# Kernel tuning notes

Measured on AMD Instinct MI355X. Metric: run time of the kernel, lower is better.

## Reference

```python
import jax, jax.numpy as jnp
import numpy as np

N, E, K = 10000, 160000, 5
K3 = K ** 3  # 125 spline kernel entries (kernel_size=5, dim=3)
NUM_CLASSES = 6890
# 8 corner combinations of the degree-1 open B-spline in 3 dims
_COMBOS = jnp.asarray(np.array([[i, j, k] for i in (0, 1) for j in (0, 1) for k in (0, 1)], dtype=np.int32))


def spline_basis(pseudo):
    # pseudo: [E,3] in [0,1]; degree-1 open B-spline, kernel_size K per dim
    p = pseudo * (K - 1)
    lo_f = jnp.floor(p)
    frac = p - lo_f                                   # [E,3]
    lo = jnp.clip(lo_f.astype(jnp.int32), 0, K - 1)    # [E,3]
    hi = jnp.minimum(lo + 1, K - 1)
    w = jnp.stack([1.0 - frac, frac], axis=-1)         # [E,3,2]
    idx = jnp.stack([lo, hi], axis=-1)                 # [E,3,2]
    c = _COMBOS                                        # [8,3]
    b = w[:, 0, c[:, 0]] * w[:, 1, c[:, 1]] * w[:, 2, c[:, 2]]          # [E,8]
    flat = idx[:, 0, c[:, 0]] + K * idx[:, 1, c[:, 1]] + K * K * idx[:, 2, c[:, 2]]  # [E,8]
    return b, flat


def spline_conv(x, src, dst, b, flat, W, root, bias):
    # x: [N,in], W: [K3,in,out], root: [in,out], bias: [out]
    xW = jnp.einsum('ni,kio->nko', x, W)               # [N,K3,out]
    gathered = xW[src[:, None], flat]                  # [E,8,out]
    msg = jnp.einsum('es,eso->eo', b, gathered)        # [E,out]
    agg = jax.ops.segment_sum(msg, dst, num_segments=N)
    deg = jax.ops.segment_sum(jnp.ones((msg.shape[0],), msg.dtype), dst, num_segments=N)
    agg = agg / jnp.maximum(deg, 1.0)[:, None]         # mean aggregation
    return agg + x @ root + bias


def setup_inputs() -> dict:
    key = jax.random.key(0)
    ks = jax.random.split(key, 24)
    s = 0.1
    x = jax.random.normal(ks[0], (N, 1), jnp.float32)
    edge_index = jax.random.randint(ks[1], (2, E), 0, N)
    pseudo = jax.random.uniform(ks[2], (E, 3), dtype=jnp.float32)
    W1 = jax.random.normal(ks[3], (K3, 1, 32), jnp.float32) * s
    root1 = jax.random.normal(ks[4], (1, 32), jnp.float32) * s
    b1 = jnp.zeros((32,), jnp.float32)
    W2 = jax.random.normal(ks[5], (K3, 32, 64), jnp.float32) * s
    root2 = jax.random.normal(ks[6], (32, 64), jnp.float32) * s
    b2 = jnp.zeros((64,), jnp.float32)
    Ws = jax.random.normal(ks[7], (4, K3, 64, 64), jnp.float32) * s  # convs 3-6
    roots = jax.random.normal(ks[8], (4, 64, 64), jnp.float32) * s
    bs = jnp.zeros((4, 64), jnp.float32)
    lin1_w = jax.random.normal(ks[9], (64, 256), jnp.float32) * s
    lin1_b = jnp.zeros((256,), jnp.float32)
    lin2_w = jax.random.normal(ks[10], (256, NUM_CLASSES), jnp.float32) * s
    lin2_b = jnp.zeros((NUM_CLASSES,), jnp.float32)
    return {'x': x, 'edge_index': edge_index, 'pseudo': pseudo,
            'W1': W1, 'root1': root1, 'b1': b1,
            'W2': W2, 'root2': root2, 'b2': b2,
            'Ws': Ws, 'roots': roots, 'bs': bs,
            'lin1_w': lin1_w, 'lin1_b': lin1_b, 'lin2_w': lin2_w, 'lin2_b': lin2_b}


def reference(x, edge_index, pseudo, W1, root1, b1, W2, root2, b2, Ws, roots, bs,
              lin1_w, lin1_b, lin2_w, lin2_b):
    src, dst = edge_index[0], edge_index[1]
    b, flat = spline_basis(pseudo)
    h = jax.nn.elu(spline_conv(x, src, dst, b, flat, W1, root1, b1))
    h = jax.nn.elu(spline_conv(h, src, dst, b, flat, W2, root2, b2))
    for l in range(4):  # convs 3-6, fixed layer loop
        h = jax.nn.elu(spline_conv(h, src, dst, b, flat, Ws[l], roots[l], bs[l]))
    h = jax.nn.elu(h @ lin1_w + lin1_b)
    # dropout is identity in eval mode
    logits = h @ lin2_w + lin2_b
    return jax.nn.log_softmax(logits, axis=-1)
```

## Files before the change

### kernel.cpp

```cpp
#include <hip/hip_runtime.h>
#include <math.h>

#define Nn 10000
#define Ee 160000
#define NPB 40
#define NBLK 250
#define NKER 125
#define NBUCK (NBLK * NKER)
#define KCHUNK 32

__global__ __launch_bounds__(256) void basis_kernel(const float* __restrict__ pseudo,
                                                    float* __restrict__ bw,
                                                    int* __restrict__ fl)
{
    int e = blockIdx.x * 256 + threadIdx.x;
    if (e >= Ee) return;
    float p0 = pseudo[e * 3 + 0] * 4.f;
    float p1 = pseudo[e * 3 + 1] * 4.f;
    float p2 = pseudo[e * 3 + 2] * 4.f;
    float f0 = floorf(p0), f1 = floorf(p1), f2 = floorf(p2);
    float fr0 = p0 - f0, fr1 = p1 - f1, fr2 = p2 - f2;
    int lo0 = (int)f0; lo0 = lo0 < 0 ? 0 : (lo0 > 4 ? 4 : lo0);
    int lo1 = (int)f1; lo1 = lo1 < 0 ? 0 : (lo1 > 4 ? 4 : lo1);
    int lo2 = (int)f2; lo2 = lo2 < 0 ? 0 : (lo2 > 4 ? 4 : lo2);
    int hi0 = lo0 + 1 > 4 ? 4 : lo0 + 1;
    int hi1 = lo1 + 1 > 4 ? 4 : lo1 + 1;
    int hi2 = lo2 + 1 > 4 ? 4 : lo2 + 1;
#pragma unroll
    for (int s = 0; s < 8; ++s) {
        int c0 = (s >> 2) & 1, c1 = (s >> 1) & 1, c2 = s & 1;
        float b = (c0 ? fr0 : 1.f - fr0) * (c1 ? fr1 : 1.f - fr1) * (c2 ? fr2 : 1.f - fr2);
        int f = (c0 ? hi0 : lo0) + 5 * (c1 ? hi1 : lo1) + 25 * (c2 ? hi2 : lo2);
        bw[e * 8 + s] = b;
        fl[e * 8 + s] = f;
    }
}

__global__ __launch_bounds__(256) void deg_kernel(const int* __restrict__ dst, int* __restrict__ degi)
{
    int e = blockIdx.x * 256 + threadIdx.x;
    if (e >= Ee) return;
    atomicAdd(&degi[dst[e]], 1);
}

__global__ __launch_bounds__(256) void invdeg_kernel(const int* __restrict__ degi, float* __restrict__ invdeg)
{
    int n = blockIdx.x * 256 + threadIdx.x;
    if (n >= Nn) return;
    int d = degi[n];
    invdeg[n] = 1.f / (float)(d > 0 ? d : 1);
}

__global__ __launch_bounds__(256) void hist_kernel(const int* __restrict__ dst, const int* __restrict__ fl,
                                                   int* __restrict__ hist)
{
    int t = blockIdx.x * 256 + threadIdx.x;
    if (t >= Ee * 8) return;
    int e = t >> 3;
    int key = (dst[e] / NPB) * NKER + fl[t];
    atomicAdd(&hist[key], 1);
}

__global__ __launch_bounds__(1024) void scan_kernel(const int* __restrict__ hist, int* __restrict__ boff)
{
    const int T = 1024;
    const int per = (NBUCK + T - 1) / T;
    int t = threadIdx.x;
    int beg = t * per;
    int end = beg + per; if (end > NBUCK) end = NBUCK;
    int s = 0;
    for (int i = beg; i < end && i < NBUCK; ++i) s += hist[i];
    __shared__ int tmp[1024];
    tmp[t] = s;
    __syncthreads();
    for (int o2 = 1; o2 < 1024; o2 <<= 1) {
        int v = (t >= o2) ? tmp[t - o2] : 0;
        __syncthreads();
        tmp[t] += v;
        __syncthreads();
    }
    int run = tmp[t] - s;
    for (int i = beg; i < end && i < NBUCK; ++i) { boff[i] = run; run += hist[i]; }
    if (t == T - 1) boff[NBUCK] = run;
}

__global__ __launch_bounds__(256) void fill_kernel(const int* __restrict__ srcA, const int* __restrict__ dstA,
                                                   const float* __restrict__ bw, const int* __restrict__ fl,
                                                   int* __restrict__ cursor, uint2* __restrict__ recs)
{
    int t = blockIdx.x * 256 + threadIdx.x;
    if (t >= Ee * 8) return;
    int e = t >> 3;
    int d = dstA[e];
    int key = (d / NPB) * NKER + fl[t];
    int pos = atomicAdd(&cursor[key], 1);
    unsigned meta = (unsigned)srcA[e] | ((unsigned)(d % NPB) << 16);
    recs[pos] = make_uint2(meta, __float_as_uint(bw[t]));
}

template <int CIN, int COUT>
__global__ __launch_bounds__(256) void conv_pairs_kernel(const uint2* __restrict__ recs,
                                                         const int* __restrict__ boff,
                                                         const float* __restrict__ xin,
                                                         const float* __restrict__ W,
                                                         float* __restrict__ agg)
{
    __shared__ float aggl[NPB * COUT];
    const int blk = blockIdx.x;
    for (int idx = threadIdx.x; idx < NPB * COUT; idx += 256) aggl[idx] = 0.f;
    __syncthreads();

    const int lane = threadIdx.x & 63;
    const int wid  = threadIdx.x >> 6;
    const int o    = lane;

    int k0 = blockIdx.y * KCHUNK;
    int k1 = k0 + KCHUNK; if (k1 > NKER) k1 = NKER;

    for (int k = k0; k < k1; ++k) {
        int bidx = blk * NKER + k;
        int pb = boff[bidx], pe = boff[bidx + 1];
        if (pb >= pe) continue;
        float wreg[CIN];
#pragma unroll
        for (int i = 0; i < CIN; ++i)
            wreg[i] = (o < COUT) ? W[(k * CIN + i) * COUT + o] : 0.f;

        for (int p = pb + wid; p < pe; p += 4) {
            uint2 r = recs[p];
            unsigned meta = (unsigned)__builtin_amdgcn_readfirstlane((int)r.x);
            float wt = __uint_as_float(r.y);
            int src = (int)(meta & 0xFFFFu);
            int dl  = (int)(meta >> 16);
            const float* xs = xin + src * CIN;
            float m0 = 0.f, m1 = 0.f, m2 = 0.f, m3 = 0.f;
            if (CIN >= 4) {
#pragma unroll
                for (int i = 0; i < CIN; i += 4) {
                    m0 += xs[i + 0] * wreg[i + 0];
                    m1 += xs[i + 1] * wreg[i + 1];
                    m2 += xs[i + 2] * wreg[i + 2];
                    m3 += xs[i + 3] * wreg[i + 3];
                }
            } else {
#pragma unroll
                for (int i = 0; i < CIN; ++i) m0 += xs[i] * wreg[i];
            }
            float m = (m0 + m1) + (m2 + m3);
            if (o < COUT) atomicAdd(&aggl[dl * COUT + o], wt * m);
        }
    }
    __syncthreads();
    for (int idx = threadIdx.x; idx < NPB * COUT; idx += 256) {
        int n = blk * NPB + idx / COUT;
        if (n < Nn) atomicAdd(&agg[n * COUT + (idx % COUT)], aggl[idx]);
    }
}

template <int CIN, int COUT>
__global__ __launch_bounds__(256) void epilogue_kernel(const float* __restrict__ agg,
                                                       const float* __restrict__ xin,
                                                       const float* __restrict__ root,
                                                       const float* __restrict__ bias,
                                                       const float* __restrict__ invdeg,
                                                       float* __restrict__ out)
{
    int idx = blockIdx.x * 256 + threadIdx.x;
    int n = idx / COUT, o = idx % COUT;
    if (n >= Nn) return;
    float r0 = 0.f, r1 = 0.f;
#pragma unroll
    for (int i = 0; i < CIN; i += 2) {
        r0 += xin[n * CIN + i] * root[i * COUT + o];
        if (CIN > 1) r1 += xin[n * CIN + i + 1] * root[(i + 1) * COUT + o];
    }
    float v = agg[n * COUT + o] * invdeg[n] + r0 + r1 + bias[o];
    out[n * COUT + o] = v > 0.f ? v : expm1f(v);
}

__global__ __launch_bounds__(256) void lin1_kernel(const float* __restrict__ h,
                                                   const float* __restrict__ w1,
                                                   const float* __restrict__ b1,
                                                   float* __restrict__ out)
{
    int n = blockIdx.x;
    __shared__ float hl[64];
    if (threadIdx.x < 64) hl[threadIdx.x] = h[n * 64 + threadIdx.x];
    __syncthreads();
    int j = threadIdx.x;
    float a0 = b1[j], a1 = 0.f, a2 = 0.f, a3 = 0.f;
#pragma unroll
    for (int i = 0; i < 64; i += 4) {
        a0 += hl[i + 0] * w1[(i + 0) * 256 + j];
        a1 += hl[i + 1] * w1[(i + 1) * 256 + j];
        a2 += hl[i + 2] * w1[(i + 2) * 256 + j];
        a3 += hl[i + 3] * w1[(i + 3) * 256 + j];
    }
    float acc = (a0 + a1) + (a2 + a3);
    out[n * 256 + j] = acc > 0.f ? acc : expm1f(acc);
}

#define LNT 32
__global__ __launch_bounds__(256) void lin2_kernel(const float* __restrict__ h,
                                                   const float* __restrict__ w2,
                                                   const float* __restrict__ b2,
                                                   float* __restrict__ out)
{
    __shared__ float hT[256 * LNT];
    int n0 = blockIdx.x * LNT;
    int j0 = blockIdx.y * 1024;
    for (int idx = threadIdx.x; idx < 256 * LNT; idx += 256) {
        int i = idx & 255, nl = idx >> 8;
        hT[i * LNT + nl] = (n0 + nl < Nn) ? h[(n0 + nl) * 256 + i] : 0.f;
    }
    __syncthreads();

    int j[4];
#pragma unroll
    for (int c = 0; c < 4; ++c) j[c] = j0 + (int)threadIdx.x + 256 * c;

    float acc[4][LNT];
#pragma unroll
    for (int c = 0; c < 4; ++c)
#pragma unroll
        for (int nl = 0; nl < LNT; ++nl) acc[c][nl] = 0.f;

    for (int i = 0; i < 256; ++i) {
        float wv[4];
#pragma unroll
        for (int c = 0; c < 4; ++c)
            wv[c] = (j[c] < 6890) ? w2[i * 6890 + j[c]] : 0.f;
        const float4* hp = (const float4*)&hT[i * LNT];
#pragma unroll
        for (int q = 0; q < LNT / 4; ++q) {
            float4 h4 = hp[q];
#pragma unroll
            for (int c = 0; c < 4; ++c) {
                acc[c][q * 4 + 0] += wv[c] * h4.x;
                acc[c][q * 4 + 1] += wv[c] * h4.y;
                acc[c][q * 4 + 2] += wv[c] * h4.z;
                acc[c][q * 4 + 3] += wv[c] * h4.w;
            }
        }
    }
#pragma unroll
    for (int c = 0; c < 4; ++c) {
        if (j[c] >= 6890) continue;
        float bb = b2[j[c]];
        for (int nl = 0; nl < LNT; ++nl) {
            int n = n0 + nl;
            if (n < Nn) out[(size_t)n * 6890 + j[c]] = acc[c][nl] + bb;
        }
    }
}

__global__ __launch_bounds__(1024) void lsm_kernel(float* __restrict__ out)
{
    int row = blockIdx.x;
    float* p = out + (size_t)row * 6890;
    __shared__ float red[16];
    int tid = threadIdx.x, lane = tid & 63, wid = tid >> 6;

    float m = -3.4e38f;
    for (int jj = tid; jj < 6890; jj += 1024) m = fmaxf(m, p[jj]);
#pragma unroll
    for (int off = 32; off > 0; off >>= 1) m = fmaxf(m, __shfl_down(m, off));
    if (lane == 0) red[wid] = m;
    __syncthreads();
    if (tid == 0) {
        float mm = red[0];
        for (int w = 1; w < 16; ++w) mm = fmaxf(mm, red[w]);
        red[0] = mm;
    }
    __syncthreads();
    m = red[0];
    __syncthreads();

    float s = 0.f;
    for (int jj = tid; jj < 6890; jj += 1024) s += expf(p[jj] - m);
#pragma unroll
    for (int off = 32; off > 0; off >>= 1) s += __shfl_down(s, off);
    if (lane == 0) red[wid] = s;
    __syncthreads();
    if (tid == 0) {
        float ss = 0.f;
        for (int w = 1; w < 16; ++w) ss += red[w];
        red[0] += ss;
    }
    __syncthreads();
    float lse = m + logf(red[0]);
    for (int jj = tid; jj < 6890; jj += 1024) p[jj] -= lse;
}

extern "C" void kernel_launch(void* const* d_in, const int* in_sizes, int n_in,
                              void* d_out, int out_size, void* d_ws, size_t ws_size,
                              hipStream_t stream)
{
    const float* x      = (const float*)d_in[0];
    const int*   ei     = (const int*)d_in[1];
    const float* pseudo = (const float*)d_in[2];
    const float* W1     = (const float*)d_in[3];
    const float* root1  = (const float*)d_in[4];
    const float* b1     = (const float*)d_in[5];
    const float* W2     = (const float*)d_in[6];
    const float* root2  = (const float*)d_in[7];
    const float* b2     = (const float*)d_in[8];
    const float* Ws     = (const float*)d_in[9];
    const float* roots  = (const float*)d_in[10];
    const float* bs     = (const float*)d_in[11];
    const float* l1w    = (const float*)d_in[12];
    const float* l1b    = (const float*)d_in[13];
    const float* l2w    = (const float*)d_in[14];
    const float* l2b    = (const float*)d_in[15];
    float* out = (float*)d_out;

    const int* srcA = ei;
    const int* dstA = ei + Ee;

    char* base = (char*)d_ws;
    size_t off = 0;
    auto carve = [&](size_t bytes) -> void* {
        void* p = base + off;
        off += (bytes + 255) & ~(size_t)255;
        return p;
    };
    float* bw     = (float*)carve((size_t)Ee * 8 * 4);
    int*   fl     = (int*)carve((size_t)Ee * 8 * 4);
    int*   hist   = (int*)carve((size_t)NBUCK * 4);
    int*   boff   = (int*)carve((size_t)(NBUCK + 1) * 4);
    int*   cursor = (int*)carve((size_t)NBUCK * 4);
    uint2* recs   = (uint2*)carve((size_t)Ee * 8 * 8);
    int*   degi   = (int*)carve((size_t)Nn * 4);
    float* invdeg = (float*)carve((size_t)Nn * 4);
    float* agg    = (float*)carve((size_t)Nn * 64 * 4);
    float* hA     = (float*)carve((size_t)Nn * 64 * 4);
    float* hB     = (float*)carve((size_t)Nn * 64 * 4);
    float* h256   = (float*)carve((size_t)Nn * 256 * 4);
    (void)ws_size; (void)n_in; (void)in_sizes; (void)out_size;

    hipMemsetAsync(hist, 0, (size_t)NBUCK * 4, stream);
    hipMemsetAsync(degi, 0, (size_t)Nn * 4, stream);

    basis_kernel<<<(Ee + 255) / 256, 256, 0, stream>>>(pseudo, bw, fl);
    deg_kernel<<<(Ee + 255) / 256, 256, 0, stream>>>(dstA, degi);
    invdeg_kernel<<<(Nn + 255) / 256, 256, 0, stream>>>(degi, invdeg);
    hist_kernel<<<(Ee * 8 + 255) / 256, 256, 0, stream>>>(dstA, fl, hist);
    scan_kernel<<<1, 1024, 0, stream>>>(hist, boff);
    hipMemcpyAsync(cursor, boff, (size_t)NBUCK * 4, hipMemcpyDeviceToDevice, stream);
    fill_kernel<<<(Ee * 8 + 255) / 256, 256, 0, stream>>>(srcA, dstA, bw, fl, cursor, recs);

    const dim3 cgrid(NBLK, (NKER + KCHUNK - 1) / KCHUNK);

    hipMemsetAsync(agg, 0, (size_t)Nn * 64 * 4, stream);
    conv_pairs_kernel<1, 32><<<cgrid, 256, 0, stream>>>(recs, boff, x, W1, agg);
    epilogue_kernel<1, 32><<<(Nn * 32 + 255) / 256, 256, 0, stream>>>(agg, x, root1, b1, invdeg, hA);

    hipMemsetAsync(agg, 0, (size_t)Nn * 64 * 4, stream);
    conv_pairs_kernel<32, 64><<<cgrid, 256, 0, stream>>>(recs, boff, hA, W2, agg);
    epilogue_kernel<32, 64><<<(Nn * 64 + 255) / 256, 256, 0, stream>>>(agg, hA, root2, b2, invdeg, hB);

    float* cin = hB;
    float* cot = hA;
    for (int l = 0; l < 4; ++l) {
        hipMemsetAsync(agg, 0, (size_t)Nn * 64 * 4, stream);
        conv_pairs_kernel<64, 64><<<cgrid, 256, 0, stream>>>(recs, boff, cin, Ws + (size_t)l * 125 * 64 * 64, agg);
        epilogue_kernel<64, 64><<<(Nn * 64 + 255) / 256, 256, 0, stream>>>(
            agg, cin, roots + (size_t)l * 64 * 64, bs + (size_t)l * 64, invdeg, cot);
        float* t = cin; cin = cot; cot = t;
    }

    lin1_kernel<<<Nn, 256, 0, stream>>>(cin, l1w, l1b, h256);
    lin2_kernel<<<dim3((Nn + LNT - 1) / LNT, 7), 256, 0, stream>>>(h256, l2w, l2b, out);
    lsm_kernel<<<Nn, 1024, 0, stream>>>(out);
}
```

Before: 3.784 ms.

## Use bf16 MFMA for final linear layer and reassign conv kernel slots per wave

```diff
diff --git a/kernel.cpp b/kernel.cpp
--- a/kernel.cpp
+++ b/kernel.cpp
@@ -1,4 +1,5 @@
 #include <hip/hip_runtime.h>
+#include <hip/hip_bf16.h>
 #include <math.h>
 
 #define Nn 10000
@@ -8,6 +9,13 @@
 #define NKER 125
 #define NBUCK (NBLK * NKER)
 #define KCHUNK 32
+
+#define MPAD 10048
+#define NPAD 6912
+#define NCLS 6890
+
+typedef short bf16x8 __attribute__((ext_vector_type(8)));
+typedef float f32x4  __attribute__((ext_vector_type(4)));
 
 __global__ __launch_bounds__(256) void basis_kernel(const float* __restrict__ pseudo,
                                                     float* __restrict__ bw,
@@ -117,7 +125,7 @@
     int k0 = blockIdx.y * KCHUNK;
     int k1 = k0 + KCHUNK; if (k1 > NKER) k1 = NKER;
 
-    for (int k = k0; k < k1; ++k) {
+    for (int k = k0 + wid; k < k1; k += 4) {
         int bidx = blk * NKER + k;
         int pb = boff[bidx], pe = boff[bidx + 1];
         if (pb >= pe) continue;
@@ -126,7 +134,7 @@
         for (int i = 0; i < CIN; ++i)
             wreg[i] = (o < COUT) ? W[(k * CIN + i) * COUT + o] : 0.f;
 
-        for (int p = pb + wid; p < pe; p += 4) {
+        for (int p = pb; p < pe; ++p) {
             uint2 r = recs[p];
             unsigned meta = (unsigned)__builtin_amdgcn_readfirstlane((int)r.x);
             float wt = __uint_as_float(r.y);
@@ -181,7 +189,7 @@
 __global__ __launch_bounds__(256) void lin1_kernel(const float* __restrict__ h,
                                                    const float* __restrict__ w1,
                                                    const float* __restrict__ b1,
-                                                   float* __restrict__ out)
+                                                   __hip_bfloat16* __restrict__ out)
 {
     int n = blockIdx.x;
     __shared__ float hl[64];
@@ -197,72 +205,92 @@
         a3 += hl[i + 3] * w1[(i + 3) * 256 + j];
     }
     float acc = (a0 + a1) + (a2 + a3);
-    out[n * 256 + j] = acc > 0.f ? acc : expm1f(acc);
-}
-
-#define LNT 32
-__global__ __launch_bounds__(256) void lin2_kernel(const float* __restrict__ h,
-                                                   const float* __restrict__ w2,
-                                                   const float* __restrict__ b2,
-                                                   float* __restrict__ out)
-{
-    __shared__ float hT[256 * LNT];
-    int n0 = blockIdx.x * LNT;
-    int j0 = blockIdx.y * 1024;
-    for (int idx = threadIdx.x; idx < 256 * LNT; idx += 256) {
-        int i = idx & 255, nl = idx >> 8;
-        hT[i * LNT + nl] = (n0 + nl < Nn) ? h[(n0 + nl) * 256 + i] : 0.f;
-    }
-    __syncthreads();
-
-    int j[4];
-#pragma unroll
-    for (int c = 0; c < 4; ++c) j[c] = j0 + (int)threadIdx.x + 256 * c;
-
-    float acc[4][LNT];
-#pragma unroll
-    for (int c = 0; c < 4; ++c)
-#pragma unroll
-        for (int nl = 0; nl < LNT; ++nl) acc[c][nl] = 0.f;
-
-    for (int i = 0; i < 256; ++i) {
-        float wv[4];
-#pragma unroll
-        for (int c = 0; c < 4; ++c)
-            wv[c] = (j[c] < 6890) ? w2[i * 6890 + j[c]] : 0.f;
-        const float4* hp = (const float4*)&hT[i * LNT];
-#pragma unroll
-        for (int q = 0; q < LNT / 4; ++q) {
-            float4 h4 = hp[q];
-#pragma unroll
-            for (int c = 0; c < 4; ++c) {
-                acc[c][q * 4 + 0] += wv[c] * h4.x;
-                acc[c][q * 4 + 1] += wv[c] * h4.y;
-                acc[c][q * 4 + 2] += wv[c] * h4.z;
-                acc[c][q * 4 + 3] += wv[c] * h4.w;
+    float v = acc > 0.f ? acc : expm1f(acc);
+    out[(size_t)n * 256 + j] = __float2bfloat16(v);
+}
+
+__global__ __launch_bounds__(256) void w2t_kernel(const float* __restrict__ w2,
+                                                  __hip_bfloat16* __restrict__ w2t)
+{
+    __shared__ float t[32][33];
+    int n0 = blockIdx.x * 32;
+    int k0 = blockIdx.y * 32;
+    int tx = threadIdx.x & 31, ty = threadIdx.x >> 5;
+#pragma unroll
+    for (int q = 0; q < 4; ++q) {
+        int k = k0 + ty + 8 * q, n = n0 + tx;
+        t[ty + 8 * q][tx] = (n < NCLS) ? w2[(size_t)k * NCLS + n] : 0.f;
+    }
+    __syncthreads();
+#pragma unroll
+    for (int q = 0; q < 4; ++q) {
+        int n = n0 + ty + 8 * q;
+        w2t[(size_t)n * 256 + k0 + tx] = __float2bfloat16(t[tx][ty + 8 * q]);
+    }
+}
+
+__global__ __launch_bounds__(256) void lin2_mfma_kernel(const __hip_bfloat16* __restrict__ hbf,
+                                                        const __hip_bfloat16* __restrict__ w2t,
+                                                        const float* __restrict__ b2,
+                                                        float* __restrict__ out)
+{
+    const int tid  = threadIdx.x;
+    const int lane = tid & 63, wid = tid >> 6;
+    const int wr = wid & 1, wc = wid >> 1;
+    const int quad = lane >> 4, lq = lane & 15;
+
+    const int mbase = blockIdx.x * 64 + wr * 32;
+    const int nbase = blockIdx.y * 128 + wc * 64;
+
+    f32x4 acc[2][4];
+#pragma unroll
+    for (int i = 0; i < 2; ++i)
+#pragma unroll
+        for (int j = 0; j < 4; ++j) acc[i][j] = (f32x4){0.f, 0.f, 0.f, 0.f};
+
+    const unsigned short* A = (const unsigned short*)hbf;
+    const unsigned short* B = (const unsigned short*)w2t;
+
+    for (int kc = 0; kc < 256; kc += 32) {
+        bf16x8 af[2], bfr[4];
+#pragma unroll
+        for (int mt = 0; mt < 2; ++mt)
+            af[mt] = *(const bf16x8*)(A + (size_t)(mbase + mt * 16 + lq) * 256 + kc + quad * 8);
+#pragma unroll
+        for (int nt = 0; nt < 4; ++nt)
+            bfr[nt] = *(const bf16x8*)(B + (size_t)(nbase + nt * 16 + lq) * 256 + kc + quad * 8);
+#pragma unroll
+        for (int mt = 0; mt < 2; ++mt)
+#pragma unroll
+            for (int nt = 0; nt < 4; ++nt)
+                acc[mt][nt] = __builtin_amdgcn_mfma_f32_16x16x32_bf16(af[mt], bfr[nt], acc[mt][nt], 0, 0, 0);
+    }
+
+#pragma unroll
+    for (int nt = 0; nt < 4; ++nt) {
+        int col = nbase + nt * 16 + lq;
+        if (col >= NCLS) continue;
+        float bb = b2[col];
+#pragma unroll
+        for (int mt = 0; mt < 2; ++mt) {
+#pragma unroll
+            for (int r = 0; r < 4; ++r) {
+                int row = mbase + mt * 16 + quad * 4 + r;
+                if (row < Nn) out[(size_t)row * NCLS + col] = acc[mt][nt][r] + bb;
             }
         }
     }
-#pragma unroll
-    for (int c = 0; c < 4; ++c) {
-        if (j[c] >= 6890) continue;
-        float bb = b2[j[c]];
-        for (int nl = 0; nl < LNT; ++nl) {
-            int n = n0 + nl;
-            if (n < Nn) out[(size_t)n * 6890 + j[c]] = acc[c][nl] + bb;
-        }
-    }
 }
 
 __global__ __launch_bounds__(1024) void lsm_kernel(float* __restrict__ out)
 {
     int row = blockIdx.x;
-    float* p = out + (size_t)row * 6890;
+    float* p = out + (size_t)row * NCLS;
     __shared__ float red[16];
     int tid = threadIdx.x, lane = tid & 63, wid = tid >> 6;
 
     float m = -3.4e38f;
-    for (int jj = tid; jj < 6890; jj += 1024) m = fmaxf(m, p[jj]);
+    for (int jj = tid; jj < NCLS; jj += 1024) m = fmaxf(m, p[jj]);
 #pragma unroll
     for (int off = 32; off > 0; off >>= 1) m = fmaxf(m, __shfl_down(m, off));
     if (lane == 0) red[wid] = m;
@@ -277,7 +305,7 @@
     __syncthreads();
 
     float s = 0.f;
-    for (int jj = tid; jj < 6890; jj += 1024) s += expf(p[jj] - m);
+    for (int jj = tid; jj < NCLS; jj += 1024) s += expf(p[jj] - m);
 #pragma unroll
     for (int off = 32; off > 0; off >>= 1) s += __shfl_down(s, off);
     if (lane == 0) red[wid] = s;
@@ -289,7 +317,7 @@
     }
     __syncthreads();
     float lse = m + logf(red[0]);
-    for (int jj = tid; jj < 6890; jj += 1024) p[jj] -= lse;
+    for (int jj = tid; jj < NCLS; jj += 1024) p[jj] -= lse;
 }
 
 extern "C" void kernel_launch(void* const* d_in, const int* in_sizes, int n_in,
@@ -335,11 +363,13 @@
     float* agg    = (float*)carve((size_t)Nn * 64 * 4);
     float* hA     = (float*)carve((size_t)Nn * 64 * 4);
     float* hB     = (float*)carve((size_t)Nn * 64 * 4);
-    float* h256   = (float*)carve((size_t)Nn * 256 * 4);
+    __hip_bfloat16* hbf = (__hip_bfloat16*)carve((size_t)MPAD * 256 * 2);
+    __hip_bfloat16* w2t = (__hip_bfloat16*)carve((size_t)NPAD * 256 * 2);
     (void)ws_size; (void)n_in; (void)in_sizes; (void)out_size;
 
     hipMemsetAsync(hist, 0, (size_t)NBUCK * 4, stream);
     hipMemsetAsync(degi, 0, (size_t)Nn * 4, stream);
+    hipMemsetAsync(hbf, 0, (size_t)MPAD * 256 * 2, stream);
 
     basis_kernel<<<(Ee + 255) / 256, 256, 0, stream>>>(pseudo, bw, fl);
     deg_kernel<<<(Ee + 255) / 256, 256, 0, stream>>>(dstA, degi);
@@ -348,6 +378,7 @@
     scan_kernel<<<1, 1024, 0, stream>>>(hist, boff);
     hipMemcpyAsync(cursor, boff, (size_t)NBUCK * 4, hipMemcpyDeviceToDevice, stream);
     fill_kernel<<<(Ee * 8 + 255) / 256, 256, 0, stream>>>(srcA, dstA, bw, fl, cursor, recs);
+    w2t_kernel<<<dim3((NPAD + 31) / 32, 8), 256, 0, stream>>>(l2w, w2t);
 
     const dim3 cgrid(NBLK, (NKER + KCHUNK - 1) / KCHUNK);
 
@@ -369,7 +400,7 @@
         float* t = cin; cin = cot; cot = t;
     }
 
-    lin1_kernel<<<Nn, 256, 0, stream>>>(cin, l1w, l1b, h256);
-    lin2_kernel<<<dim3((Nn + LNT - 1) / LNT, 7), 256, 0, stream>>>(h256, l2w, l2b, out);
+    lin1_kernel<<<Nn, 256, 0, stream>>>(cin, l1w, l1b, hbf);
+    lin2_mfma_kernel<<<dim3(MPAD / 64, NPAD / 128), 256, 0, stream>>>(hbf, w2t, l2b, out);
     lsm_kernel<<<Nn, 1024, 0, stream>>>(out);
 }
```

Measured after the change: 3.483 ms. 1.09x faster.
